# Optimization experiments

Hardware: AMD Instinct MI355X
Metric: run time of the kernel (lower is better)

Reference implementation:

```python
import jax, jax.numpy as jnp
import numpy as np

# Concrete segmented-polynomial instance (uniform 1d):
N = 8192      # nodes (rows of input 0 and of the indexed output)
E = 16384     # edges (batch dim of input 1 and of the per-edge product)
S = 16        # segments per operand (buffer_num_segments, same for all 3 operands)
EXT = 64      # operand_extent (uniform segment shape)
P = 2048      # num_paths of the single operation


def setup_inputs() -> dict:
    key = jax.random.key(0)
    k0, k1, k2, k3, k4, k5 = jax.random.split(key, 6)
    x = jax.random.normal(k0, (N, S * EXT), dtype=jnp.float32)          # node features
    y = jax.random.normal(k1, (E, S * EXT), dtype=jnp.float32)          # edge features
    idx_in = jax.random.randint(k2, (E,), 0, N, dtype=jnp.int32)        # gather index for input 0
    idx_out = jax.random.randint(k3, (E,), 0, N, dtype=jnp.int32)       # scatter index for output 0
    path_indices = jax.random.randint(k4, (P, 3), 0, S, dtype=jnp.int32)  # (i_x, j_y, k_out) per path
    path_coefficients = jax.random.normal(k5, (P,), dtype=jnp.float32)
    return {
        "x": x, "y": y,
        "idx_in": idx_in, "idx_out": idx_out,
        "path_indices": path_indices,
        "path_coefficients": path_coefficients,
    }


def reference(x, y, idx_in, idx_out, path_indices, path_coefficients):
    # Dense path-coefficient tensor C[k, i, j]: duplicate paths accumulate,
    # missing (k,i,j) triples are zero. This is the math-dtype (fp32) contraction
    # the uniform-1d kernel performs over segments of equal extent.
    C = jnp.zeros((S, S, S), dtype=x.dtype).at[
        path_indices[:, 2], path_indices[:, 0], path_indices[:, 1]
    ].add(path_coefficients)

    xr = x.reshape(N, S, EXT)[idx_in]   # gather (BATCH_DIM_INDEXED input): [E, S, EXT]
    yr = y.reshape(E, S, EXT)           # batched input:                    [E, S, EXT]

    # out_e[e, k, c] = sum_{i,j} C[k,i,j] * xr[e,i,c] * yr[e,j,c]
    out_e = jnp.einsum('kij,eic,ejc->ekc', C, xr, yr)

    # scatter-add (BATCH_DIM_INDEXED output) into N output rows
    out = jnp.zeros((N, S, EXT), dtype=x.dtype).at[idx_out].add(out_e)
    return out.reshape(N, S * EXT)
```

## Files before the change

### kernel.cpp

```cpp
#include <hip/hip_runtime.h>
#include <hip/hip_bf16.h>

#define N_NODES 8192
#define E_EDGES 16384
#define S_SEG   16
#define EXT     64
#define P_PATHS 2048
#define ROW     1024
#define L_SLOTS 8
#define NWAVES  (E_EDGES / L_SLOTS)
#define NBLK    (NWAVES / 4)

typedef _Float16 f16x8  __attribute__((ext_vector_type(8)));
typedef _Float16 f16x4  __attribute__((ext_vector_type(4)));
typedef _Float16 half2v __attribute__((ext_vector_type(2)));
typedef float    f32x4  __attribute__((ext_vector_type(4)));

#define WS_CMAT  0
#define WS_HIST  8192
#define WS_CURS  40960
#define WS_ROWS  73728
#define WS_ELIST 106512
#define WS_XRS   172048
#define WS_NDS   237584

__global__ void prep(const int* __restrict__ pidx, const float* __restrict__ pcoef,
                     _Float16* __restrict__ Cmat, int* __restrict__ hist) {
    const int tid = threadIdx.x;
    if (blockIdx.x < 32) { hist[blockIdx.x * 256 + tid] = 0; return; }
    __shared__ float sC[S_SEG * S_SEG * S_SEG];
    for (int i = tid; i < 4096; i += 256) sC[i] = 0.f;
    __syncthreads();
    for (int p = tid; p < P_PATHS; p += 256) {
        int i = pidx[3 * p + 0];
        int j = pidx[3 * p + 1];
        int k = pidx[3 * p + 2];
        atomicAdd(&sC[(k * S_SEG + i) * S_SEG + j], pcoef[p]);
    }
    __syncthreads();
    for (int i = tid; i < 4096; i += 256) Cmat[i] = (_Float16)sC[i];
}

__global__ void hist_k(const int* __restrict__ idx_out, int* __restrict__ hist) {
    const int e = blockIdx.x * 256 + threadIdx.x;
    atomicAdd(&hist[idx_out[e]], 1);
}

__global__ __launch_bounds__(256) void scan_k(const int* __restrict__ hist,
                                              int* __restrict__ rows,
                                              int* __restrict__ cursor) {
    __shared__ int part[256];
    const int t = threadIdx.x;
    const int base = t * 32;
    int loc[32];
    int s = 0;
#pragma unroll
    for (int i = 0; i < 32; ++i) { loc[i] = s; s += hist[base + i]; }
    part[t] = s;
    __syncthreads();
    for (int off = 1; off < 256; off <<= 1) {
        int v = part[t];
        int u = (t >= off) ? part[t - off] : 0;
        __syncthreads();
        part[t] = v + u;
        __syncthreads();
    }
    const int excl = (t == 0) ? 0 : part[t - 1];
#pragma unroll
    for (int i = 0; i < 32; ++i) {
        int v = excl + loc[i];
        rows[base + i] = v;
        cursor[base + i] = v;
    }
    if (t == 255) rows[N_NODES] = part[255];
}

__global__ void scatter_k(const int* __restrict__ idx_in, const int* __restrict__ idx_out,
                          int* __restrict__ cursor, int* __restrict__ elist,
                          int* __restrict__ xrs, int* __restrict__ nds) {
    const int e = blockIdx.x * 256 + threadIdx.x;
    const int nd = idx_out[e];
    const int pos = atomicAdd(&cursor[nd], 1);
    elist[pos] = e;
    xrs[pos]   = idx_in[e];
    nds[pos]   = nd;
}

__global__ __launch_bounds__(256) void zerofill_k(const int* __restrict__ rows,
                                                  float* __restrict__ out) {
    const int n = blockIdx.x * 4 + (threadIdx.x >> 6);
    const int lane = threadIdx.x & 63;
    const int beg = rows[n], end = rows[n + 1];
    const bool need = (beg == end) || ((beg / L_SLOTS) != ((end - 1) / L_SLOTS));
    if (!need) return;
    const float4 z = {0.f, 0.f, 0.f, 0.f};
    float* ob = out + (size_t)n * ROW + lane * 4;
#pragma unroll
    for (int r = 0; r < 4; ++r) *(float4*)(ob + r * 256) = z;
}

__global__ __launch_bounds__(256) void seg_poly_slots(
        const float* __restrict__ x, const float* __restrict__ y,
        const _Float16* __restrict__ Cmat,
        const int* __restrict__ elist, const int* __restrict__ xrs,
        const int* __restrict__ nds, float* __restrict__ out) {
    __shared__ __attribute__((aligned(16))) _Float16 sx_all[4][ROW];
    __shared__ __attribute__((aligned(16))) half2v   sy_all[4][512];

    const int tid  = threadIdx.x;
    const int lane = tid & 63;
    const int wv   = tid >> 6;
    _Float16* sxh = sx_all[wv];
    half2v*   syp = sy_all[wv];

    const int wid = blockIdx.x * 4 + wv;
    const int s0  = wid * L_SLOTS;

    const int quad = lane >> 4;
    const int m    = lane & 15;
    const int jb2  = (quad & 1) * 4;
    const int ih   = quad >> 1;
    const int jp   = lane >> 3;
    const int cq   = (lane & 7) * 8;

    int e_[L_SLOTS], xr_[L_SLOTS], nd_[L_SLOTS];
    {
        int4 a = *(const int4*)(elist + s0); int4 b = *(const int4*)(elist + s0 + 4);
        e_[0]=a.x; e_[1]=a.y; e_[2]=a.z; e_[3]=a.w; e_[4]=b.x; e_[5]=b.y; e_[6]=b.z; e_[7]=b.w;
        a = *(const int4*)(xrs + s0); b = *(const int4*)(xrs + s0 + 4);
        xr_[0]=a.x; xr_[1]=a.y; xr_[2]=a.z; xr_[3]=a.w; xr_[4]=b.x; xr_[5]=b.y; xr_[6]=b.z; xr_[7]=b.w;
        a = *(const int4*)(nds + s0); b = *(const int4*)(nds + s0 + 4);
        nd_[0]=a.x; nd_[1]=a.y; nd_[2]=a.z; nd_[3]=a.w; nd_[4]=b.x; nd_[5]=b.y; nd_[6]=b.z; nd_[7]=b.w;
    }
    const bool prev_same = (s0 > 0)                  && (nds[s0 - 1]       == nd_[0]);
    const bool next_same = (s0 + L_SLOTS < E_EDGES)  && (nds[s0 + L_SLOTS] == nd_[L_SLOTS - 1]);

    f16x8 afrag[8];
    {
        const _Float16* basep = Cmat + m * 256 + quad * 8;
#pragma unroll
        for (int kk = 0; kk < 8; ++kk) afrag[kk] = *(const f16x8*)(basep + kk * 32);
    }

    float4 xbuf[2][4], ybuf[2][4];
    auto issue = [&](int t, int b) {
        const float* xp = x + (size_t)xr_[t] * ROW;
        const float* yp = y + (size_t)e_[t] * ROW;
#pragma unroll
        for (int k4 = 0; k4 < 4; ++k4)
            xbuf[b][k4] = *(const float4*)(xp + k4 * 256 + lane * 4);
        ybuf[b][0] = *(const float4*)(yp + (2 * jp)     * EXT + cq);
        ybuf[b][1] = *(const float4*)(yp + (2 * jp)     * EXT + cq + 4);
        ybuf[b][2] = *(const float4*)(yp + (2 * jp + 1) * EXT + cq);
        ybuf[b][3] = *(const float4*)(yp + (2 * jp + 1) * EXT + cq + 4);
    };
    issue(0, 0);

    f32x4 acc[4];
#pragma unroll
    for (int ct = 0; ct < 4; ++ct) acc[ct] = f32x4{0.f, 0.f, 0.f, 0.f};
    int segStart = 0;

#pragma unroll
    for (int t = 0; t < L_SLOTS; ++t) {
        const int b = t & 1;
        if (t + 1 < L_SLOTS) issue(t + 1, b ^ 1);

#pragma unroll
        for (int k4 = 0; k4 < 4; ++k4) {
            const float4 v = xbuf[b][k4];
            *(f16x4*)(sxh + k4 * 256 + lane * 4) =
                f16x4{(_Float16)v.x, (_Float16)v.y, (_Float16)v.z, (_Float16)v.w};
        }
        {
            const float4 a0 = ybuf[b][0], a1 = ybuf[b][1];
            const float4 c0 = ybuf[b][2], c1 = ybuf[b][3];
            *(f16x8*)(syp + jp * 64 + cq) =
                f16x8{(_Float16)a0.x, (_Float16)c0.x, (_Float16)a0.y, (_Float16)c0.y,
                      (_Float16)a0.z, (_Float16)c0.z, (_Float16)a0.w, (_Float16)c0.w};
            *(f16x8*)(syp + jp * 64 + cq + 4) =
                f16x8{(_Float16)a1.x, (_Float16)c1.x, (_Float16)a1.y, (_Float16)c1.y,
                      (_Float16)a1.z, (_Float16)c1.z, (_Float16)a1.w, (_Float16)c1.w};
        }

#pragma unroll
        for (int ct = 0; ct < 4; ++ct) {
            const int c = ct * 16 + m;
            half2v ypk[4];
#pragma unroll
            for (int r = 0; r < 4; ++r) ypk[r] = syp[(jb2 + r) * 64 + c];
#pragma unroll
            for (int kk = 0; kk < 8; ++kk) {
                const _Float16 xh = sxh[(2 * kk + ih) * EXT + c];
                const half2v hx = {xh, xh};
                const half2v b0 = hx * ypk[0];
                const half2v b1 = hx * ypk[1];
                const half2v b2 = hx * ypk[2];
                const half2v b3 = hx * ypk[3];
                const f16x8 bfrag = {b0[0], b0[1], b1[0], b1[1],
                                     b2[0], b2[1], b3[0], b3[1]};
                acc[ct] = __builtin_amdgcn_mfma_f32_16x16x32_f16(
                              afrag[kk], bfrag, acc[ct], 0, 0, 0);
            }
        }

        const bool last = (t == L_SLOTS - 1);
        if (last || nd_[t + 1] != nd_[t]) {
            const bool shared = (segStart == 0 && prev_same) || (last && next_same);
            float* ob = out + (size_t)nd_[t] * ROW;
            if (shared) {
#pragma unroll
                for (int ct = 0; ct < 4; ++ct)
#pragma unroll
                    for (int r = 0; r < 4; ++r)
                        atomicAdd(ob + (quad * 4 + r) * EXT + ct * 16 + m, acc[ct][r]);
            } else {
#pragma unroll
                for (int ct = 0; ct < 4; ++ct)
#pragma unroll
                    for (int r = 0; r < 4; ++r)
                        ob[(quad * 4 + r) * EXT + ct * 16 + m] = acc[ct][r];
            }
#pragma unroll
            for (int ct = 0; ct < 4; ++ct) acc[ct] = f32x4{0.f, 0.f, 0.f, 0.f};
            segStart = t + 1;
        }
    }
}

extern "C" void kernel_launch(void* const* d_in, const int* in_sizes, int n_in,
                              void* d_out, int out_size, void* d_ws, size_t ws_size,
                              hipStream_t stream) {
    const float* x       = (const float*)d_in[0];
    const float* y       = (const float*)d_in[1];
    const int*   idx_in  = (const int*)d_in[2];
    const int*   idx_out = (const int*)d_in[3];
    const int*   pidx    = (const int*)d_in[4];
    const float* pcoef   = (const float*)d_in[5];
    float* out           = (float*)d_out;

    char* ws = (char*)d_ws;
    _Float16* Cmat = (_Float16*)(ws + WS_CMAT);
    int* hist      = (int*)(ws + WS_HIST);
    int* cursor    = (int*)(ws + WS_CURS);
    int* rows      = (int*)(ws + WS_ROWS);
    int* elist     = (int*)(ws + WS_ELIST);
    int* xrs       = (int*)(ws + WS_XRS);
    int* nds       = (int*)(ws + WS_NDS);

    prep<<<33, 256, 0, stream>>>(pidx, pcoef, Cmat, hist);
    hist_k<<<E_EDGES / 256, 256, 0, stream>>>(idx_out, hist);
    scan_k<<<1, 256, 0, stream>>>(hist, rows, cursor);
    scatter_k<<<E_EDGES / 256, 256, 0, stream>>>(idx_in, idx_out, cursor, elist, xrs, nds);
    zerofill_k<<<N_NODES / 4, 256, 0, stream>>>(rows, out);
    seg_poly_slots<<<NBLK, 256, 0, stream>>>(x, y, Cmat, elist, xrs, nds, out);
}
```

Measured before the change: 162.2 us.

## Load x/y rows straight into LDS asynchronously and build fp16 operands from fp32

```diff
diff --git a/kernel.cpp b/kernel.cpp
--- a/kernel.cpp
+++ b/kernel.cpp
@@ -12,9 +12,17 @@
 #define NBLK    (NWAVES / 4)
 
 typedef _Float16 f16x8  __attribute__((ext_vector_type(8)));
-typedef _Float16 f16x4  __attribute__((ext_vector_type(4)));
 typedef _Float16 half2v __attribute__((ext_vector_type(2)));
 typedef float    f32x4  __attribute__((ext_vector_type(4)));
+
+#define PKRTZ(a, b) __builtin_bit_cast(half2v, __builtin_amdgcn_cvt_pkrtz((a), (b)))
+
+#define GLOAD16(gp, lp)                                                  \
+    __builtin_amdgcn_global_load_lds(                                    \
+        (const __attribute__((address_space(1))) void*)(gp),             \
+        (__attribute__((address_space(3))) void*)(lp), 16, 0, 0)
+
+#define WAIT_VMCNT(n) asm volatile("s_waitcnt vmcnt(" #n ")" ::: "memory")
 
 #define WS_CMAT  0
 #define WS_HIST  8192
@@ -93,35 +101,31 @@
     const int beg = rows[n], end = rows[n + 1];
     const bool need = (beg == end) || ((beg / L_SLOTS) != ((end - 1) / L_SLOTS));
     if (!need) return;
-    const float4 z = {0.f, 0.f, 0.f, 0.f};
+    const f32x4 z = {0.f, 0.f, 0.f, 0.f};
     float* ob = out + (size_t)n * ROW + lane * 4;
 #pragma unroll
-    for (int r = 0; r < 4; ++r) *(float4*)(ob + r * 256) = z;
-}
-
-__global__ __launch_bounds__(256) void seg_poly_slots(
+    for (int r = 0; r < 4; ++r)
+        __builtin_nontemporal_store(z, (f32x4*)(ob + r * 256));
+}
+
+__global__ __launch_bounds__(256) void seg_poly_async(
         const float* __restrict__ x, const float* __restrict__ y,
         const _Float16* __restrict__ Cmat,
         const int* __restrict__ elist, const int* __restrict__ xrs,
         const int* __restrict__ nds, float* __restrict__ out) {
-    __shared__ __attribute__((aligned(16))) _Float16 sx_all[4][ROW];
-    __shared__ __attribute__((aligned(16))) half2v   sy_all[4][512];
+    __shared__ __attribute__((aligned(16))) float sbuf[4][2][2048];
 
     const int tid  = threadIdx.x;
     const int lane = tid & 63;
     const int wv   = tid >> 6;
-    _Float16* sxh = sx_all[wv];
-    half2v*   syp = sy_all[wv];
 
     const int wid = blockIdx.x * 4 + wv;
     const int s0  = wid * L_SLOTS;
 
     const int quad = lane >> 4;
     const int m    = lane & 15;
-    const int jb2  = (quad & 1) * 4;
     const int ih   = quad >> 1;
-    const int jp   = lane >> 3;
-    const int cq   = (lane & 7) * 8;
+    const int jb   = (quad & 1) * 8;
 
     int e_[L_SLOTS], xr_[L_SLOTS], nd_[L_SLOTS];
     {
@@ -132,8 +136,8 @@
         a = *(const int4*)(nds + s0); b = *(const int4*)(nds + s0 + 4);
         nd_[0]=a.x; nd_[1]=a.y; nd_[2]=a.z; nd_[3]=a.w; nd_[4]=b.x; nd_[5]=b.y; nd_[6]=b.z; nd_[7]=b.w;
     }
-    const bool prev_same = (s0 > 0)                  && (nds[s0 - 1]       == nd_[0]);
-    const bool next_same = (s0 + L_SLOTS < E_EDGES)  && (nds[s0 + L_SLOTS] == nd_[L_SLOTS - 1]);
+    const bool prev_same = (s0 > 0)                 && (nds[s0 - 1]       == nd_[0]);
+    const bool next_same = (s0 + L_SLOTS < E_EDGES) && (nds[s0 + L_SLOTS] == nd_[L_SLOTS - 1]);
 
     f16x8 afrag[8];
     {
@@ -142,19 +146,19 @@
         for (int kk = 0; kk < 8; ++kk) afrag[kk] = *(const f16x8*)(basep + kk * 32);
     }
 
-    float4 xbuf[2][4], ybuf[2][4];
     auto issue = [&](int t, int b) {
         const float* xp = x + (size_t)xr_[t] * ROW;
         const float* yp = y + (size_t)e_[t] * ROW;
-#pragma unroll
-        for (int k4 = 0; k4 < 4; ++k4)
-            xbuf[b][k4] = *(const float4*)(xp + k4 * 256 + lane * 4);
-        ybuf[b][0] = *(const float4*)(yp + (2 * jp)     * EXT + cq);
-        ybuf[b][1] = *(const float4*)(yp + (2 * jp)     * EXT + cq + 4);
-        ybuf[b][2] = *(const float4*)(yp + (2 * jp + 1) * EXT + cq);
-        ybuf[b][3] = *(const float4*)(yp + (2 * jp + 1) * EXT + cq + 4);
+        float* lx = &sbuf[wv][b][0];
+        float* ly = &sbuf[wv][b][1024];
+#pragma unroll
+        for (int k4 = 0; k4 < 4; ++k4) {
+            GLOAD16(xp + k4 * 256 + lane * 4, lx + k4 * 256);
+            GLOAD16(yp + k4 * 256 + lane * 4, ly + k4 * 256);
+        }
     };
     issue(0, 0);
+    issue(1, 1);
 
     f32x4 acc[4];
 #pragma unroll
@@ -164,41 +168,29 @@
 #pragma unroll
     for (int t = 0; t < L_SLOTS; ++t) {
         const int b = t & 1;
-        if (t + 1 < L_SLOTS) issue(t + 1, b ^ 1);
-
-#pragma unroll
-        for (int k4 = 0; k4 < 4; ++k4) {
-            const float4 v = xbuf[b][k4];
-            *(f16x4*)(sxh + k4 * 256 + lane * 4) =
-                f16x4{(_Float16)v.x, (_Float16)v.y, (_Float16)v.z, (_Float16)v.w};
-        }
-        {
-            const float4 a0 = ybuf[b][0], a1 = ybuf[b][1];
-            const float4 c0 = ybuf[b][2], c1 = ybuf[b][3];
-            *(f16x8*)(syp + jp * 64 + cq) =
-                f16x8{(_Float16)a0.x, (_Float16)c0.x, (_Float16)a0.y, (_Float16)c0.y,
-                      (_Float16)a0.z, (_Float16)c0.z, (_Float16)a0.w, (_Float16)c0.w};
-            *(f16x8*)(syp + jp * 64 + cq + 4) =
-                f16x8{(_Float16)a1.x, (_Float16)c1.x, (_Float16)a1.y, (_Float16)c1.y,
-                      (_Float16)a1.z, (_Float16)c1.z, (_Float16)a1.w, (_Float16)c1.w};
-        }
+        if (t + 1 < L_SLOTS) { WAIT_VMCNT(8); } else { WAIT_VMCNT(0); }
+
+        const float* sX = &sbuf[wv][b][0];
+        const float* sY = &sbuf[wv][b][1024];
 
 #pragma unroll
         for (int ct = 0; ct < 4; ++ct) {
             const int c = ct * 16 + m;
-            half2v ypk[4];
-#pragma unroll
-            for (int r = 0; r < 4; ++r) ypk[r] = syp[(jb2 + r) * 64 + c];
+            float y0[4], y1[4];
+#pragma unroll
+            for (int r = 0; r < 4; ++r) {
+                y0[r] = sY[(jb + 2 * r) * 64 + c];
+                y1[r] = sY[(jb + 2 * r + 1) * 64 + c];
+            }
 #pragma unroll
             for (int kk = 0; kk < 8; ++kk) {
-                const _Float16 xh = sxh[(2 * kk + ih) * EXT + c];
-                const half2v hx = {xh, xh};
-                const half2v b0 = hx * ypk[0];
-                const half2v b1 = hx * ypk[1];
-                const half2v b2 = hx * ypk[2];
-                const half2v b3 = hx * ypk[3];
-                const f16x8 bfrag = {b0[0], b0[1], b1[0], b1[1],
-                                     b2[0], b2[1], b3[0], b3[1]};
+                const float xf = sX[(2 * kk + ih) * 64 + c];
+                const half2v h0 = PKRTZ(xf * y0[0], xf * y1[0]);
+                const half2v h1 = PKRTZ(xf * y0[1], xf * y1[1]);
+                const half2v h2 = PKRTZ(xf * y0[2], xf * y1[2]);
+                const half2v h3 = PKRTZ(xf * y0[3], xf * y1[3]);
+                const f16x8 bfrag = {h0[0], h0[1], h1[0], h1[1],
+                                     h2[0], h2[1], h3[0], h3[1]};
                 acc[ct] = __builtin_amdgcn_mfma_f32_16x16x32_f16(
                               afrag[kk], bfrag, acc[ct], 0, 0, 0);
             }
@@ -219,12 +211,15 @@
                 for (int ct = 0; ct < 4; ++ct)
 #pragma unroll
                     for (int r = 0; r < 4; ++r)
-                        ob[(quad * 4 + r) * EXT + ct * 16 + m] = acc[ct][r];
+                        __builtin_nontemporal_store(
+                            acc[ct][r], ob + (quad * 4 + r) * EXT + ct * 16 + m);
             }
 #pragma unroll
             for (int ct = 0; ct < 4; ++ct) acc[ct] = f32x4{0.f, 0.f, 0.f, 0.f};
             segStart = t + 1;
         }
+
+        if (t + 2 < L_SLOTS) issue(t + 2, b);
     }
 }
 
@@ -253,5 +248,5 @@
     scan_k<<<1, 256, 0, stream>>>(hist, rows, cursor);
     scatter_k<<<E_EDGES / 256, 256, 0, stream>>>(idx_in, idx_out, cursor, elist, xrs, nds);
     zerofill_k<<<N_NODES / 4, 256, 0, stream>>>(rows, out);
-    seg_poly_slots<<<NBLK, 256, 0, stream>>>(x, y, Cmat, elist, xrs, nds, out);
-}
+    seg_poly_async<<<NBLK, 256, 0, stream>>>(x, y, Cmat, elist, xrs, nds, out);
+}
```

After: 166.0 us. +2.4%, slower.
